# Kernel optimization log

Measured on AMD Instinct MI355X. Metric: run time of the kernel, lower is better.

## Reference

```python
import jax, jax.numpy as jnp
import numpy as np

N = 50000
E = 1000000
WIDTH = 64
DEPTH = 4


def setup_inputs() -> dict:
    key = jax.random.key(0)
    ks = jax.random.split(key, 6)
    x = jax.random.normal(ks[0], (N, 5), dtype=jnp.float32)
    edge_index = jax.random.randint(ks[1], (2, E), 0, N, dtype=jnp.int32)
    edge_attr = jax.random.normal(ks[2], (E, 3), dtype=jnp.float32)
    w1 = jax.random.normal(ks[3], (3, WIDTH), dtype=jnp.float32) / jnp.sqrt(3.0)
    b1 = jnp.zeros((WIDTH,), jnp.float32)
    w2 = jax.random.normal(ks[4], (WIDTH, 1), dtype=jnp.float32) / jnp.sqrt(float(WIDTH))
    b2 = jnp.zeros((1,), jnp.float32)
    root = jax.random.normal(ks[5], (1, 1), dtype=jnp.float32)
    bias = jnp.zeros((1,), jnp.float32)
    return dict(x=x, edge_index=edge_index, edge_attr=edge_attr,
                w1=w1, b1=b1, w2=w2, b2=b2, root=root, bias=bias)


def reference(x, edge_index, edge_attr, w1, b1, w2, b2, root, bias):
    # h: scalar node feature, column 2 of data.x -> [N, 1]
    h = x[:, 2:3]
    src, dst = edge_index[0], edge_index[1]  # messages flow src -> dst

    # Per-edge 1x1 weight from the edge MLP (depends only on edge_attr,
    # identical for all depth iterations since the conv is shared).
    w_e = jax.nn.relu(edge_attr @ w1 + b1) @ w2 + b2  # [E, 1]

    # Mean aggregation: precompute in-degree of each target node.
    deg = jax.ops.segment_sum(jnp.ones((E,), jnp.float32), dst, num_segments=N)
    inv_deg = jnp.where(deg > 0, 1.0 / jnp.maximum(deg, 1.0), 0.0)[:, None]  # [N, 1]

    for _ in range(DEPTH):
        msg = h[src] * w_e                                        # gather + per-edge weight, [E, 1]
        agg = jax.ops.segment_sum(msg, dst, num_segments=N) * inv_deg  # scatter-mean, [N, 1]
        h = jax.nn.relu(agg + h @ root + bias)                    # root transform + bias + ReLU
    return h
```

## Files before the change

kernel.cpp:

```cpp
#include <hip/hip_runtime.h>

#define NN 50000
#define NE 1000000
#define NBK 196
#define EPB 1024
#define PB 977
#define ESTRIDE 5632

__global__ void init_fixed(const float* __restrict__ x, float* __restrict__ h,
                           int* __restrict__ cursor, int* __restrict__ sBeg,
                           int* __restrict__ sLim) {
    int i = blockIdx.x * 256 + threadIdx.x;
    if (i < NN) h[i] = x[5 * i + 2];
    if (i < NBK) {
        cursor[i] = i * ESTRIDE;
        sBeg[i]   = i * ESTRIDE;
        sLim[i]   = (i + 1) * ESTRIDE;
    }
}

__global__ void bucket_count(const int* __restrict__ dst, int* __restrict__ bcnt,
                             const float* __restrict__ x, float* __restrict__ h) {
    __shared__ int hist[NBK];
    int t = threadIdx.x;
    if (t < NBK) hist[t] = 0;
    __syncthreads();
    int gid = blockIdx.x * 256 + t;
    if (gid < NN) h[gid] = x[5 * gid + 2];
#pragma unroll
    for (int j = 0; j < 4; ++j) {
        int e = blockIdx.x * EPB + j * 256 + t;
        if (e < NE) atomicAdd(&hist[dst[e] >> 8], 1);
    }
    __syncthreads();
    if (t < NBK && hist[t]) atomicAdd(&bcnt[t], hist[t]);
}

__global__ void bucket_scan(const int* __restrict__ bcnt,
                            int* __restrict__ sBeg,
                            int* __restrict__ cursor,
                            int* __restrict__ sLim) {
    __shared__ int part[256];
    int t = threadIdx.x;
    int v = (t < NBK) ? ((bcnt[t] + 1) & ~1) : 0;
    part[t] = v;
    __syncthreads();
    for (int off = 1; off < 256; off <<= 1) {
        int x = part[t];
        int add = (t >= off) ? part[t - off] : 0;
        __syncthreads();
        part[t] = x + add;
        __syncthreads();
    }
    if (t < NBK) {
        int excl = part[t] - v;
        sBeg[t] = excl;
        cursor[t] = excl;
        sLim[t] = 0x7FFFFFFF;
    }
}

__global__ void place_kernel(const float* __restrict__ ea,
                             const int* __restrict__ src,
                             const int* __restrict__ dst,
                             const float* __restrict__ w1,
                             const float* __restrict__ b1,
                             const float* __restrict__ w2,
                             const float* __restrict__ b2,
                             const int* __restrict__ sLim,
                             int* __restrict__ cursor,
                             uint2* __restrict__ es,
                             int dumpbase) {
    __shared__ float sw1[192];
    __shared__ float sb1[64];
    __shared__ float sw2[64];
    __shared__ int hist[NBK];
    __shared__ int hbase[NBK];
    int t = threadIdx.x;
    if (t < 192) sw1[t] = w1[t];
    if (t < 64) { sb1[t] = b1[t]; sw2[t] = w2[t]; }
    if (t < NBK) hist[t] = 0;
    __syncthreads();

    int r[4], dd[4], ss[4];
    float ce[4];
#pragma unroll
    for (int j = 0; j < 4; ++j) {
        int e = blockIdx.x * EPB + j * 256 + t;
        dd[j] = -1;
        if (e < NE) {
            float a0 = ea[3 * e + 0];
            float a1 = ea[3 * e + 1];
            float a2 = ea[3 * e + 2];
            float c0 = b2[0], c1 = 0.f, c2 = 0.f, c3 = 0.f;
#pragma unroll
            for (int k = 0; k < 64; k += 4) {
                float h0 = fmaf(a0, sw1[k+0], fmaf(a1, sw1[64+k+0], fmaf(a2, sw1[128+k+0], sb1[k+0])));
                float h1 = fmaf(a0, sw1[k+1], fmaf(a1, sw1[64+k+1], fmaf(a2, sw1[128+k+1], sb1[k+1])));
                float h2 = fmaf(a0, sw1[k+2], fmaf(a1, sw1[64+k+2], fmaf(a2, sw1[128+k+2], sb1[k+2])));
                float h3 = fmaf(a0, sw1[k+3], fmaf(a1, sw1[64+k+3], fmaf(a2, sw1[128+k+3], sb1[k+3])));
                c0 = fmaf(fmaxf(h0, 0.f), sw2[k+0], c0);
                c1 = fmaf(fmaxf(h1, 0.f), sw2[k+1], c1);
                c2 = fmaf(fmaxf(h2, 0.f), sw2[k+2], c2);
                c3 = fmaf(fmaxf(h3, 0.f), sw2[k+3], c3);
            }
            ce[j] = (c0 + c1) + (c2 + c3);
            ss[j] = src[e];
            int d = dst[e];
            dd[j] = d;
            r[j] = atomicAdd(&hist[d >> 8], 1);
        }
    }
    __syncthreads();
    if (t < NBK) { int hv = hist[t]; if (hv) hbase[t] = atomicAdd(&cursor[t], hv); }
    __syncthreads();
#pragma unroll
    for (int j = 0; j < 4; ++j) {
        int e = blockIdx.x * EPB + j * 256 + t;
        if (e < NE) {
            int d = dd[j];
            int b = d >> 8;
            int pos = hbase[b] + r[j];
            if (pos >= sLim[b]) pos = dumpbase + (t & 63);
            unsigned pack = (unsigned)ss[j] | ((unsigned)(d & 255) << 17);
            es[pos] = make_uint2(pack, __float_as_uint(ce[j]));
        }
    }
}

template<int FIRST>
__global__ __launch_bounds__(1024)
void round_fused(const int* __restrict__ sBeg,
                 const int* __restrict__ sEnd,
                 const int* __restrict__ sLim,
                 const uint2* __restrict__ es,
                 const float* __restrict__ hold,
                 float* __restrict__ hnew,
                 float* __restrict__ invdeg,
                 const float* __restrict__ root,
                 const float* __restrict__ bias) {
    __shared__ float lagg[256];
    __shared__ int ldeg[256];
    int t = threadIdx.x;
    int b = blockIdx.x;
    if (t < 256) { lagg[t] = 0.f; if (FIRST) ldeg[t] = 0; }
    __syncthreads();
    int s0 = sBeg[b];
    int s1 = sEnd[b];
    { int cap = sLim[b]; if (s1 > cap) s1 = cap; }
    const uint4* es4 = (const uint4*)es;
    for (int p = s0 + t * 2; p < s1; p += 2048) {
        uint4 v = es4[p >> 1];
        {
            int sidx = v.x & 0x1FFFF;
            int dl = (v.x >> 17) & 255;
            atomicAdd(&lagg[dl], hold[sidx] * __uint_as_float(v.y));
            if (FIRST) atomicAdd(&ldeg[dl], 1);
        }
        if (p + 1 < s1) {
            int sidx = v.z & 0x1FFFF;
            int dl = (v.z >> 17) & 255;
            atomicAdd(&lagg[dl], hold[sidx] * __uint_as_float(v.w));
            if (FIRST) atomicAdd(&ldeg[dl], 1);
        }
    }
    __syncthreads();
    if (t < 256) {
        int node = b * 256 + t;
        if (node < NN) {
            float inv;
            if (FIRST) {
                int d = ldeg[t];
                inv = (d > 0) ? (1.0f / (float)d) : 0.f;
                invdeg[node] = inv;
            } else {
                inv = invdeg[node];
            }
            float a = lagg[t];
            hnew[node] = fmaxf(fmaf(hold[node], root[0], fmaf(a, inv, bias[0])), 0.f);
        }
    }
}


extern "C" void kernel_launch(void* const* d_in, const int* in_sizes, int n_in,
                              void* d_out, int out_size, void* d_ws, size_t ws_size,
                              hipStream_t stream) {
    const float* x    = (const float*)d_in[0];
    const int*   ei   = (const int*)d_in[1];
    const float* ea   = (const float*)d_in[2];
    const float* w1   = (const float*)d_in[3];
    const float* b1   = (const float*)d_in[4];
    const float* w2   = (const float*)d_in[5];
    const float* b2   = (const float*)d_in[6];
    const float* root = (const float*)d_in[7];
    const float* bias = (const float*)d_in[8];

    const int* src = ei;
    const int* dst = ei + NE;
    float* h = (float*)d_out;

    const int BLK = 256;

    const size_t esFixed = (size_t)NBK * ESTRIDE + 64;
    const size_t needFixed = esFixed * 8
                           + (size_t)(NBK * 3) * 4
                           + (size_t)NN * 4 * 2;

    if (ws_size >= needFixed) {
        uint2* es     = (uint2*)d_ws;
        int*   cursor = (int*)(es + esFixed);
        int*   sBeg   = cursor + NBK;
        int*   sLim   = sBeg + NBK;
        float* invdeg = (float*)(sLim + NBK);
        float* hB     = invdeg + NN;

        init_fixed<<<NBK, BLK, 0, stream>>>(x, h, cursor, sBeg, sLim);
        place_kernel<<<PB, BLK, 0, stream>>>(ea, src, dst, w1, b1, w2, b2,
                                             sLim, cursor, es, (int)(NBK * ESTRIDE));
        round_fused<1><<<NBK, 1024, 0, stream>>>(sBeg, cursor, sLim, es, h,  hB, invdeg, root, bias);
        round_fused<0><<<NBK, 1024, 0, stream>>>(sBeg, cursor, sLim, es, hB, h,  invdeg, root, bias);
        round_fused<0><<<NBK, 1024, 0, stream>>>(sBeg, cursor, sLim, es, h,  hB, invdeg, root, bias);
        round_fused<0><<<NBK, 1024, 0, stream>>>(sBeg, cursor, sLim, es, hB, h,  invdeg, root, bias);
    } else {
        uint2* es     = (uint2*)d_ws;
        int*   bcnt   = (int*)(es + NE + NBK);
        int*   cursor = bcnt + NBK;
        int*   sBeg   = cursor + NBK;
        int*   sLim   = sBeg + NBK;
        float* invdeg = (float*)(sLim + NBK);
        float* hB     = invdeg + NN;

        hipMemsetAsync(bcnt, 0, NBK * 4, stream);
        bucket_count<<<PB, BLK, 0, stream>>>(dst, bcnt, x, h);
        bucket_scan<<<1, 256, 0, stream>>>(bcnt, sBeg, cursor, sLim);
        place_kernel<<<PB, BLK, 0, stream>>>(ea, src, dst, w1, b1, w2, b2,
                                             sLim, cursor, es, 0);
        round_fused<1><<<NBK, 1024, 0, stream>>>(sBeg, cursor, sLim, es, h,  hB, invdeg, root, bias);
        round_fused<0><<<NBK, 1024, 0, stream>>>(sBeg, cursor, sLim, es, hB, h,  invdeg, root, bias);
        round_fused<0><<<NBK, 1024, 0, stream>>>(sBeg, cursor, sLim, es, h,  hB, invdeg, root, bias);
        round_fused<0><<<NBK, 1024, 0, stream>>>(sBeg, cursor, sLim, es, hB, h,  invdeg, root, bias);
    }
}
```

Baseline: 151.3 us.

## Fuse init, placement and four rounds into one cooperative persistent kernel

Replaces the six-launch fixed-stride path with a single cooperative kernel of 256 blocks x 1024 threads. It uses grid.sync between the init, edge-placement and propagation phases. Each block keeps its bucket's edge records in registers across all four rounds, so they are loaded once, and it keeps the inverse degree in a register. This removes launch gaps and repeated edge-stream reads, at the cost of grid-wide barriers and lower parallelism in the placement phase (256 blocks instead of 977).

```diff
diff --git a/kernel.cpp b/kernel.cpp
--- a/kernel.cpp
+++ b/kernel.cpp
@@ -1,21 +1,155 @@
 #include <hip/hip_runtime.h>
+#include <hip/hip_cooperative_groups.h>
+
+namespace cg = cooperative_groups;
 
 #define NN 50000
 #define NE 1000000
 #define NBK 196
+#define ESTRIDE 5632
+#define MB 256
+#define MT 1024
+#define EPBM 4096
+
 #define EPB 1024
 #define PB 977
-#define ESTRIDE 5632
-
-__global__ void init_fixed(const float* __restrict__ x, float* __restrict__ h,
-                           int* __restrict__ cursor, int* __restrict__ sBeg,
-                           int* __restrict__ sLim) {
-    int i = blockIdx.x * 256 + threadIdx.x;
-    if (i < NN) h[i] = x[5 * i + 2];
-    if (i < NBK) {
-        cursor[i] = i * ESTRIDE;
-        sBeg[i]   = i * ESTRIDE;
-        sLim[i]   = (i + 1) * ESTRIDE;
+
+__global__ __launch_bounds__(MT)
+void mega(const float* __restrict__ x,
+          const int* __restrict__ src,
+          const int* __restrict__ dst,
+          const float* __restrict__ ea,
+          const float* __restrict__ w1,
+          const float* __restrict__ b1,
+          const float* __restrict__ w2,
+          const float* __restrict__ b2,
+          const float* __restrict__ root,
+          const float* __restrict__ bias,
+          int* __restrict__ cursor,
+          uint2* __restrict__ es,
+          float* __restrict__ hA,
+          float* __restrict__ hB,
+          float* __restrict__ out) {
+    cg::grid_group grid = cg::this_grid();
+    __shared__ float sw1[192];
+    __shared__ float sb1[64];
+    __shared__ float sw2[64];
+    __shared__ int   hist[NBK];
+    __shared__ int   hbase[NBK];
+    __shared__ float lagg[256];
+    __shared__ int   ldeg[256];
+    const int t = threadIdx.x;
+    const int bid = blockIdx.x;
+
+    {
+        int i = bid * MT + t;
+        if (i < NN) hA[i] = x[5 * i + 2];
+    }
+    if (bid == 0 && t < NBK) cursor[t] = t * ESTRIDE;
+    if (t < 192) sw1[t] = w1[t];
+    if (t < 64) { sb1[t] = b1[t]; sw2[t] = w2[t]; }
+    if (t < NBK) hist[t] = 0;
+    const float rt = root[0], bs = bias[0], bz = b2[0];
+    grid.sync();
+
+    {
+        int dd[4], r[4];
+        float ce[4];
+#pragma unroll
+        for (int j = 0; j < 4; ++j) {
+            int e = bid * EPBM + j * MT + t;
+            dd[j] = -1;
+            if (e < NE) {
+                float a0 = ea[3 * e + 0];
+                float a1 = ea[3 * e + 1];
+                float a2 = ea[3 * e + 2];
+                float c0 = bz, c1 = 0.f, c2 = 0.f, c3 = 0.f;
+#pragma unroll
+                for (int k = 0; k < 64; k += 4) {
+                    float h0 = fmaf(a0, sw1[k+0], fmaf(a1, sw1[64+k+0], fmaf(a2, sw1[128+k+0], sb1[k+0])));
+                    float h1 = fmaf(a0, sw1[k+1], fmaf(a1, sw1[64+k+1], fmaf(a2, sw1[128+k+1], sb1[k+1])));
+                    float h2 = fmaf(a0, sw1[k+2], fmaf(a1, sw1[64+k+2], fmaf(a2, sw1[128+k+2], sb1[k+2])));
+                    float h3 = fmaf(a0, sw1[k+3], fmaf(a1, sw1[64+k+3], fmaf(a2, sw1[128+k+3], sb1[k+3])));
+                    c0 = fmaf(fmaxf(h0, 0.f), sw2[k+0], c0);
+                    c1 = fmaf(fmaxf(h1, 0.f), sw2[k+1], c1);
+                    c2 = fmaf(fmaxf(h2, 0.f), sw2[k+2], c2);
+                    c3 = fmaf(fmaxf(h3, 0.f), sw2[k+3], c3);
+                }
+                ce[j] = (c0 + c1) + (c2 + c3);
+                int d = dst[e];
+                dd[j] = d;
+                r[j] = atomicAdd(&hist[d >> 8], 1);
+            }
+        }
+        __syncthreads();
+        if (t < NBK) { int hv = hist[t]; if (hv) hbase[t] = atomicAdd(&cursor[t], hv); }
+        __syncthreads();
+#pragma unroll
+        for (int j = 0; j < 4; ++j) {
+            int e = bid * EPBM + j * MT + t;
+            if (dd[j] >= 0) {
+                int d = dd[j];
+                int b = d >> 8;
+                int pos = hbase[b] + r[j];
+                if (pos >= (b + 1) * ESTRIDE) pos = NBK * ESTRIDE + (t & 63);
+                unsigned pack = (unsigned)src[e] | ((unsigned)(d & 255) << 17);
+                es[pos] = make_uint2(pack, __float_as_uint(ce[j]));
+            }
+        }
+    }
+    grid.sync();
+
+    const int b = bid;
+    const bool act = (b < NBK);
+    const int node = b * 256 + t;
+    const uint4* es4 = (const uint4*)es;
+    uint4 v0, v1, v2;
+    bool m0 = false, n0 = false, m1 = false, n1 = false, m2 = false, n2 = false;
+    float inv = 0.f;
+    const float* hc = hA;
+    float* hn = hB;
+
+    for (int rr = 0; rr < 4; ++rr) {
+        if (act) {
+            if (t < 256) { lagg[t] = 0.f; if (rr == 0) ldeg[t] = 0; }
+            __syncthreads();
+            if (rr == 0) {
+                int s0 = b * ESTRIDE;
+                int s1 = cursor[b];
+                int cap = s0 + ESTRIDE;
+                if (s1 > cap) s1 = cap;
+                int p0 = s0 + t * 2;
+                m0 = (p0        < s1); n0 = (p0 + 1    < s1);
+                m1 = (p0 + 2048 < s1); n1 = (p0 + 2049 < s1);
+                m2 = (p0 + 4096 < s1); n2 = (p0 + 4097 < s1);
+                if (m0) v0 = es4[p0 >> 1];
+                if (m1) v1 = es4[(p0 + 2048) >> 1];
+                if (m2) v2 = es4[(p0 + 4096) >> 1];
+            }
+            float ho = 0.f;
+            if (t < 256 && node < NN) ho = hc[node];
+            float g0a = 0.f, g0b = 0.f, g1a = 0.f, g1b = 0.f, g2a = 0.f, g2b = 0.f;
+            if (m0) g0a = hc[v0.x & 0x1FFFF];
+            if (n0) g0b = hc[v0.z & 0x1FFFF];
+            if (m1) g1a = hc[v1.x & 0x1FFFF];
+            if (n1) g1b = hc[v1.z & 0x1FFFF];
+            if (m2) g2a = hc[v2.x & 0x1FFFF];
+            if (n2) g2b = hc[v2.z & 0x1FFFF];
+            if (m0) { atomicAdd(&lagg[(v0.x >> 17) & 255], g0a * __uint_as_float(v0.y)); if (rr == 0) atomicAdd(&ldeg[(v0.x >> 17) & 255], 1); }
+            if (n0) { atomicAdd(&lagg[(v0.z >> 17) & 255], g0b * __uint_as_float(v0.w)); if (rr == 0) atomicAdd(&ldeg[(v0.z >> 17) & 255], 1); }
+            if (m1) { atomicAdd(&lagg[(v1.x >> 17) & 255], g1a * __uint_as_float(v1.y)); if (rr == 0) atomicAdd(&ldeg[(v1.x >> 17) & 255], 1); }
+            if (n1) { atomicAdd(&lagg[(v1.z >> 17) & 255], g1b * __uint_as_float(v1.w)); if (rr == 0) atomicAdd(&ldeg[(v1.z >> 17) & 255], 1); }
+            if (m2) { atomicAdd(&lagg[(v2.x >> 17) & 255], g2a * __uint_as_float(v2.y)); if (rr == 0) atomicAdd(&ldeg[(v2.x >> 17) & 255], 1); }
+            if (n2) { atomicAdd(&lagg[(v2.z >> 17) & 255], g2b * __uint_as_float(v2.w)); if (rr == 0) atomicAdd(&ldeg[(v2.z >> 17) & 255], 1); }
+            __syncthreads();
+            if (t < 256 && node < NN) {
+                if (rr == 0) { int d = ldeg[t]; inv = (d > 0) ? (1.0f / (float)d) : 0.f; }
+                float* w = (rr == 3) ? out : hn;
+                w[node] = fmaxf(fmaf(ho, rt, fmaf(lagg[t], inv, bs)), 0.f);
+            }
+        }
+        if (rr < 3) grid.sync();
+        const float* tmp = hc; hc = hn; hn = (float*)tmp;
     }
 }
 
@@ -74,6 +208,7 @@
     __shared__ float sw1[192];
     __shared__ float sb1[64];
     __shared__ float sw2[64];
+    __shared__ float sce[EPB];
     __shared__ int hist[NBK];
     __shared__ int hbase[NBK];
     int t = threadIdx.x;
@@ -82,8 +217,7 @@
     if (t < NBK) hist[t] = 0;
     __syncthreads();
 
-    int r[4], dd[4], ss[4];
-    float ce[4];
+    int r[4], dd[4];
 #pragma unroll
     for (int j = 0; j < 4; ++j) {
         int e = blockIdx.x * EPB + j * 256 + t;
@@ -104,8 +238,7 @@
                 c2 = fmaf(fmaxf(h2, 0.f), sw2[k+2], c2);
                 c3 = fmaf(fmaxf(h3, 0.f), sw2[k+3], c3);
             }
-            ce[j] = (c0 + c1) + (c2 + c3);
-            ss[j] = src[e];
+            sce[j * 256 + t] = (c0 + c1) + (c2 + c3);
             int d = dst[e];
             dd[j] = d;
             r[j] = atomicAdd(&hist[d >> 8], 1);
@@ -122,8 +255,8 @@
             int b = d >> 8;
             int pos = hbase[b] + r[j];
             if (pos >= sLim[b]) pos = dumpbase + (t & 63);
-            unsigned pack = (unsigned)ss[j] | ((unsigned)(d & 255) << 17);
-            es[pos] = make_uint2(pack, __float_as_uint(ce[j]));
+            unsigned pack = (unsigned)src[e] | ((unsigned)(d & 255) << 17);
+            es[pos] = make_uint2(pack, __float_as_uint(sce[j * 256 + t]));
         }
     }
 }
@@ -176,8 +309,7 @@
             } else {
                 inv = invdeg[node];
             }
-            float a = lagg[t];
-            hnew[node] = fmaxf(fmaf(hold[node], root[0], fmaf(a, inv, bias[0])), 0.f);
+            hnew[node] = fmaxf(fmaf(hold[node], root[0], fmaf(lagg[t], inv, bias[0])), 0.f);
         }
     }
 }
@@ -198,30 +330,26 @@
 
     const int* src = ei;
     const int* dst = ei + NE;
-    float* h = (float*)d_out;
-
-    const int BLK = 256;
+    float* out = (float*)d_out;
 
     const size_t esFixed = (size_t)NBK * ESTRIDE + 64;
     const size_t needFixed = esFixed * 8
-                           + (size_t)(NBK * 3) * 4
+                           + (size_t)NBK * 4
                            + (size_t)NN * 4 * 2;
 
     if (ws_size >= needFixed) {
         uint2* es     = (uint2*)d_ws;
         int*   cursor = (int*)(es + esFixed);
-        int*   sBeg   = cursor + NBK;
-        int*   sLim   = sBeg + NBK;
-        float* invdeg = (float*)(sLim + NBK);
-        float* hB     = invdeg + NN;
-
-        init_fixed<<<NBK, BLK, 0, stream>>>(x, h, cursor, sBeg, sLim);
-        place_kernel<<<PB, BLK, 0, stream>>>(ea, src, dst, w1, b1, w2, b2,
-                                             sLim, cursor, es, (int)(NBK * ESTRIDE));
-        round_fused<1><<<NBK, 1024, 0, stream>>>(sBeg, cursor, sLim, es, h,  hB, invdeg, root, bias);
-        round_fused<0><<<NBK, 1024, 0, stream>>>(sBeg, cursor, sLim, es, hB, h,  invdeg, root, bias);
-        round_fused<0><<<NBK, 1024, 0, stream>>>(sBeg, cursor, sLim, es, h,  hB, invdeg, root, bias);
-        round_fused<0><<<NBK, 1024, 0, stream>>>(sBeg, cursor, sLim, es, hB, h,  invdeg, root, bias);
+        float* hA     = (float*)(cursor + NBK);
+        float* hB     = hA + NN;
+
+        void* args[] = {
+            (void*)&x, (void*)&src, (void*)&dst, (void*)&ea,
+            (void*)&w1, (void*)&b1, (void*)&w2, (void*)&b2,
+            (void*)&root, (void*)&bias,
+            (void*)&cursor, (void*)&es, (void*)&hA, (void*)&hB, (void*)&out
+        };
+        hipLaunchCooperativeKernel((void*)mega, dim3(MB), dim3(MT), args, 0, stream);
     } else {
         uint2* es     = (uint2*)d_ws;
         int*   bcnt   = (int*)(es + NE + NBK);
@@ -230,7 +358,9 @@
         int*   sLim   = sBeg + NBK;
         float* invdeg = (float*)(sLim + NBK);
         float* hB     = invdeg + NN;
-
+        float* h      = out;
+
+        const int BLK = 256;
         hipMemsetAsync(bcnt, 0, NBK * 4, stream);
         bucket_count<<<PB, BLK, 0, stream>>>(dst, bcnt, x, h);
         bucket_scan<<<1, 256, 0, stream>>>(bcnt, sBeg, cursor, sLim);
```

Measured after the change: 301.1 us. +99.1%, slower.

## Sub-bucket edges by source block so gathers read h from LDS

Applied to the files above, without the earlier changes.

Adds a reorder pass that sorts each destination bucket's edges by source block of 256 nodes. Each edge is repacked as (local src, local dst, weight), and the per-sub-bucket end offsets are recorded. The new round kernel has each wave stage one source block of h in shared memory and gather from there, with prefetch of the next block. The aim is to replace random global gathers of h with LDS reads. In exchange it adds a reorder kernel, a second edge buffer, and a serial 196-step loop per block. The h buffers are padded because of the float4 loads.

```diff
diff --git a/kernel.cpp b/kernel.cpp
--- a/kernel.cpp
+++ b/kernel.cpp
@@ -1,62 +1,22 @@
 #include <hip/hip_runtime.h>
 
 #define NN 50000
+#define NNP 50176
 #define NE 1000000
 #define NBK 196
 #define EPB 1024
 #define PB 977
 #define ESTRIDE 5632
 
-__global__ void init_fixed(const float* __restrict__ x, float* __restrict__ h,
+__global__ void init_fixed(const float* __restrict__ x, float* __restrict__ hA,
                            int* __restrict__ cursor, int* __restrict__ sBeg,
                            int* __restrict__ sLim) {
     int i = blockIdx.x * 256 + threadIdx.x;
-    if (i < NN) h[i] = x[5 * i + 2];
+    if (i < NN) hA[i] = x[5 * i + 2];
     if (i < NBK) {
         cursor[i] = i * ESTRIDE;
         sBeg[i]   = i * ESTRIDE;
         sLim[i]   = (i + 1) * ESTRIDE;
-    }
-}
-
-__global__ void bucket_count(const int* __restrict__ dst, int* __restrict__ bcnt,
-                             const float* __restrict__ x, float* __restrict__ h) {
-    __shared__ int hist[NBK];
-    int t = threadIdx.x;
-    if (t < NBK) hist[t] = 0;
-    __syncthreads();
-    int gid = blockIdx.x * 256 + t;
-    if (gid < NN) h[gid] = x[5 * gid + 2];
-#pragma unroll
-    for (int j = 0; j < 4; ++j) {
-        int e = blockIdx.x * EPB + j * 256 + t;
-        if (e < NE) atomicAdd(&hist[dst[e] >> 8], 1);
-    }
-    __syncthreads();
-    if (t < NBK && hist[t]) atomicAdd(&bcnt[t], hist[t]);
-}
-
-__global__ void bucket_scan(const int* __restrict__ bcnt,
-                            int* __restrict__ sBeg,
-                            int* __restrict__ cursor,
-                            int* __restrict__ sLim) {
-    __shared__ int part[256];
-    int t = threadIdx.x;
-    int v = (t < NBK) ? ((bcnt[t] + 1) & ~1) : 0;
-    part[t] = v;
-    __syncthreads();
-    for (int off = 1; off < 256; off <<= 1) {
-        int x = part[t];
-        int add = (t >= off) ? part[t - off] : 0;
-        __syncthreads();
-        part[t] = x + add;
-        __syncthreads();
-    }
-    if (t < NBK) {
-        int excl = part[t] - v;
-        sBeg[t] = excl;
-        cursor[t] = excl;
-        sLim[t] = 0x7FFFFFFF;
     }
 }
 
@@ -74,6 +34,7 @@
     __shared__ float sw1[192];
     __shared__ float sb1[64];
     __shared__ float sw2[64];
+    __shared__ float sce[EPB];
     __shared__ int hist[NBK];
     __shared__ int hbase[NBK];
     int t = threadIdx.x;
@@ -82,8 +43,7 @@
     if (t < NBK) hist[t] = 0;
     __syncthreads();
 
-    int r[4], dd[4], ss[4];
-    float ce[4];
+    int r[4], dd[4];
 #pragma unroll
     for (int j = 0; j < 4; ++j) {
         int e = blockIdx.x * EPB + j * 256 + t;
@@ -104,8 +64,7 @@
                 c2 = fmaf(fmaxf(h2, 0.f), sw2[k+2], c2);
                 c3 = fmaf(fmaxf(h3, 0.f), sw2[k+3], c3);
             }
-            ce[j] = (c0 + c1) + (c2 + c3);
-            ss[j] = src[e];
+            sce[j * 256 + t] = (c0 + c1) + (c2 + c3);
             int d = dst[e];
             dd[j] = d;
             r[j] = atomicAdd(&hist[d >> 8], 1);
@@ -122,9 +81,189 @@
             int b = d >> 8;
             int pos = hbase[b] + r[j];
             if (pos >= sLim[b]) pos = dumpbase + (t & 63);
-            unsigned pack = (unsigned)ss[j] | ((unsigned)(d & 255) << 17);
-            es[pos] = make_uint2(pack, __float_as_uint(ce[j]));
-        }
+            unsigned pack = (unsigned)src[e] | ((unsigned)(d & 255) << 17);
+            es[pos] = make_uint2(pack, __float_as_uint(sce[j * 256 + t]));
+        }
+    }
+}
+
+__global__ __launch_bounds__(1024)
+void reorder_kernel(const int* __restrict__ cursor,
+                    const uint2* __restrict__ es,
+                    uint2* __restrict__ es2,
+                    int* __restrict__ pEnd) {
+    __shared__ int hist[256];
+    __shared__ int part[256];
+    __shared__ int cur[NBK];
+    int t = threadIdx.x;
+    int b = blockIdx.x;
+    if (t < 256) hist[t] = 0;
+    __syncthreads();
+    int s0 = b * ESTRIDE;
+    int cap = s0 + ESTRIDE;
+    int s1 = cursor[b];
+    if (s1 > cap) s1 = cap;
+
+    uint2 v[6]; int sg[6]; bool mv[6];
+#pragma unroll
+    for (int k = 0; k < 6; ++k) {
+        int p = s0 + k * 1024 + t;
+        mv[k] = (p < s1);
+        if (mv[k]) {
+            v[k] = es[p];
+            sg[k] = (v[k].x >> 8) & 0x1FF;
+            atomicAdd(&hist[sg[k]], 1);
+        }
+    }
+    __syncthreads();
+    int val = 0;
+    if (t < 256) { val = hist[t]; part[t] = val; }
+    __syncthreads();
+    for (int off = 1; off < 256; off <<= 1) {
+        int xv = 0, add = 0;
+        if (t < 256) { xv = part[t]; if (t >= off) add = part[t - off]; }
+        __syncthreads();
+        if (t < 256) part[t] = xv + add;
+        __syncthreads();
+    }
+    if (t < NBK) cur[t] = s0 + part[t] - val;
+    __syncthreads();
+#pragma unroll
+    for (int k = 0; k < 6; ++k) {
+        if (mv[k]) {
+            int pos = atomicAdd(&cur[sg[k]], 1);
+            if (pos >= cap) pos = NBK * ESTRIDE + (t & 63);
+            unsigned pk = (v[k].x & 255u) | (((v[k].x >> 17) & 255u) << 8);
+            es2[pos] = make_uint2(pk, v[k].y);
+        }
+    }
+    __syncthreads();
+    if (t < NBK) pEnd[b * NBK + t] = cur[t];
+}
+
+template<int FIRST>
+__global__ __launch_bounds__(1024)
+void round2(const int* __restrict__ pEnd,
+            const uint2* __restrict__ es2,
+            const float* __restrict__ hold,
+            float* __restrict__ hnew,
+            float* __restrict__ invdeg,
+            const float* __restrict__ root,
+            const float* __restrict__ bias) {
+    __shared__ float sh[16][256];
+    __shared__ float lagg[256];
+    __shared__ int ldeg[256];
+    int t = threadIdx.x;
+    int b = blockIdx.x;
+    int lane = t & 63, w = t >> 6;
+    float ho = 0.f;
+    int node = b * 256 + t;
+    if (t < 256) {
+        lagg[t] = 0.f;
+        if (FIRST) ldeg[t] = 0;
+        if (node < NN) ho = hold[node];
+    }
+    __syncthreads();
+
+    const float4* h4 = (const float4*)hold;
+    const int pb = b * NBK;
+    const int base0 = b * ESTRIDE;
+    const int cap = base0 + ESTRIDE;
+    float* shw = &sh[w][0];
+
+    int s = w;
+    float4 hv = h4[s * 64 + lane];
+    int beg = (s == 0) ? base0 : pEnd[pb + s - 1];
+    int end = pEnd[pb + s];
+    if (beg > cap) beg = cap;
+    if (end > cap) end = cap;
+    uint2 ev; bool evm = (beg + lane < end);
+    if (evm) ev = es2[beg + lane];
+
+    while (s < NBK) {
+        int ns = s + 16;
+        float4 nhv; int nbeg = 0, nend = 0; uint2 nev; bool nevm = false;
+        if (ns < NBK) {
+            nhv = h4[ns * 64 + lane];
+            nbeg = pEnd[pb + ns - 1];
+            nend = pEnd[pb + ns];
+            if (nbeg > cap) nbeg = cap;
+            if (nend > cap) nend = cap;
+            nevm = (nbeg + lane < nend);
+            if (nevm) nev = es2[nbeg + lane];
+        }
+        shw[lane * 4 + 0] = hv.x;
+        shw[lane * 4 + 1] = hv.y;
+        shw[lane * 4 + 2] = hv.z;
+        shw[lane * 4 + 3] = hv.w;
+        if (evm) {
+            float hs = shw[ev.x & 255];
+            int dl = (ev.x >> 8) & 255;
+            atomicAdd(&lagg[dl], hs * __uint_as_float(ev.y));
+            if (FIRST) atomicAdd(&ldeg[dl], 1);
+        }
+        for (int p = beg + lane + 64; p < end; p += 64) {
+            uint2 vv = es2[p];
+            float hs = shw[vv.x & 255];
+            int dl = (vv.x >> 8) & 255;
+            atomicAdd(&lagg[dl], hs * __uint_as_float(vv.y));
+            if (FIRST) atomicAdd(&ldeg[dl], 1);
+        }
+        s = ns; hv = nhv; beg = nbeg; end = nend; ev = nev; evm = nevm;
+    }
+    __syncthreads();
+
+    if (t < 256 && node < NN) {
+        float inv;
+        if (FIRST) {
+            int d = ldeg[t];
+            inv = (d > 0) ? (1.0f / (float)d) : 0.f;
+            invdeg[node] = inv;
+        } else {
+            inv = invdeg[node];
+        }
+        hnew[node] = fmaxf(fmaf(ho, root[0], fmaf(lagg[t], inv, bias[0])), 0.f);
+    }
+}
+
+__global__ void bucket_count(const int* __restrict__ dst, int* __restrict__ bcnt,
+                             const float* __restrict__ x, float* __restrict__ h) {
+    __shared__ int hist[NBK];
+    int t = threadIdx.x;
+    if (t < NBK) hist[t] = 0;
+    __syncthreads();
+    int gid = blockIdx.x * 256 + t;
+    if (gid < NN) h[gid] = x[5 * gid + 2];
+#pragma unroll
+    for (int j = 0; j < 4; ++j) {
+        int e = blockIdx.x * EPB + j * 256 + t;
+        if (e < NE) atomicAdd(&hist[dst[e] >> 8], 1);
+    }
+    __syncthreads();
+    if (t < NBK && hist[t]) atomicAdd(&bcnt[t], hist[t]);
+}
+
+__global__ void bucket_scan(const int* __restrict__ bcnt,
+                            int* __restrict__ sBeg,
+                            int* __restrict__ cursor,
+                            int* __restrict__ sLim) {
+    __shared__ int part[256];
+    int t = threadIdx.x;
+    int v = (t < NBK) ? ((bcnt[t] + 1) & ~1) : 0;
+    part[t] = v;
+    __syncthreads();
+    for (int off = 1; off < 256; off <<= 1) {
+        int x = part[t];
+        int add = (t >= off) ? part[t - off] : 0;
+        __syncthreads();
+        part[t] = x + add;
+        __syncthreads();
+    }
+    if (t < NBK) {
+        int excl = part[t] - v;
+        sBeg[t] = excl;
+        cursor[t] = excl;
+        sLim[t] = 0x7FFFFFFF;
     }
 }
 
@@ -176,8 +315,7 @@
             } else {
                 inv = invdeg[node];
             }
-            float a = lagg[t];
-            hnew[node] = fmaxf(fmaf(hold[node], root[0], fmaf(a, inv, bias[0])), 0.f);
+            hnew[node] = fmaxf(fmaf(hold[node], root[0], fmaf(lagg[t], inv, bias[0])), 0.f);
         }
     }
 }
@@ -198,30 +336,36 @@
 
     const int* src = ei;
     const int* dst = ei + NE;
-    float* h = (float*)d_out;
+    float* out = (float*)d_out;
 
     const int BLK = 256;
-
-    const size_t esFixed = (size_t)NBK * ESTRIDE + 64;
-    const size_t needFixed = esFixed * 8
+    const int gN = (NN + BLK - 1) / BLK;
+
+    const size_t esN = (size_t)NBK * ESTRIDE + 64;
+    const size_t needFixed = esN * 8 * 2
+                           + (size_t)(NBK * NBK) * 4
                            + (size_t)(NBK * 3) * 4
-                           + (size_t)NN * 4 * 2;
+                           + (size_t)NNP * 4 * 3;
 
     if (ws_size >= needFixed) {
         uint2* es     = (uint2*)d_ws;
-        int*   cursor = (int*)(es + esFixed);
+        uint2* es2    = es + esN;
+        int*   pEnd   = (int*)(es2 + esN);
+        int*   cursor = pEnd + NBK * NBK;
         int*   sBeg   = cursor + NBK;
         int*   sLim   = sBeg + NBK;
         float* invdeg = (float*)(sLim + NBK);
-        float* hB     = invdeg + NN;
-
-        init_fixed<<<NBK, BLK, 0, stream>>>(x, h, cursor, sBeg, sLim);
+        float* hA     = invdeg + NNP;
+        float* hB     = hA + NNP;
+
+        init_fixed<<<NBK, BLK, 0, stream>>>(x, hA, cursor, sBeg, sLim);
         place_kernel<<<PB, BLK, 0, stream>>>(ea, src, dst, w1, b1, w2, b2,
                                              sLim, cursor, es, (int)(NBK * ESTRIDE));
-        round_fused<1><<<NBK, 1024, 0, stream>>>(sBeg, cursor, sLim, es, h,  hB, invdeg, root, bias);
-        round_fused<0><<<NBK, 1024, 0, stream>>>(sBeg, cursor, sLim, es, hB, h,  invdeg, root, bias);
-        round_fused<0><<<NBK, 1024, 0, stream>>>(sBeg, cursor, sLim, es, h,  hB, invdeg, root, bias);
-        round_fused<0><<<NBK, 1024, 0, stream>>>(sBeg, cursor, sLim, es, hB, h,  invdeg, root, bias);
+        reorder_kernel<<<NBK, 1024, 0, stream>>>(cursor, es, es2, pEnd);
+        round2<1><<<NBK, 1024, 0, stream>>>(pEnd, es2, hA, hB, invdeg, root, bias);
+        round2<0><<<NBK, 1024, 0, stream>>>(pEnd, es2, hB, hA, invdeg, root, bias);
+        round2<0><<<NBK, 1024, 0, stream>>>(pEnd, es2, hA, hB, invdeg, root, bias);
+        round2<0><<<NBK, 1024, 0, stream>>>(pEnd, es2, hB, out, invdeg, root, bias);
     } else {
         uint2* es     = (uint2*)d_ws;
         int*   bcnt   = (int*)(es + NE + NBK);
@@ -230,6 +374,7 @@
         int*   sLim   = sBeg + NBK;
         float* invdeg = (float*)(sLim + NBK);
         float* hB     = invdeg + NN;
+        float* h      = out;
 
         hipMemsetAsync(bcnt, 0, NBK * 4, stream);
         bucket_count<<<PB, BLK, 0, stream>>>(dst, bcnt, x, h);
```

Result: slower. 167.4 us (+10.7%).
